# Optimization experiments

Hardware: AMD Instinct MI355X
Metric: run time of the kernel (lower is better)

The kernel has to match this reference:

```python
import jax, jax.numpy as jnp
import numpy as np
import math

D_MODEL = 1024
NUM_HEADS = 16
N_GROUP = 4
HEAD_DIM = D_MODEL // NUM_HEADS  # 64
KV_DIM = N_GROUP * HEAD_DIM      # 256
BS, SEQ = 2, 2048


def setup_inputs() -> dict:
    key = jax.random.key(0)
    ks = jax.random.split(key, 7)
    s = 0.02
    return {
        "h": jax.random.normal(ks[0], (BS, SEQ, D_MODEL), dtype=jnp.float32),
        "wq_w": jax.random.normal(ks[1], (D_MODEL, D_MODEL), dtype=jnp.float32) * s,
        "wq_b": jnp.zeros((D_MODEL,), dtype=jnp.float32),
        "wk_w": jax.random.normal(ks[2], (KV_DIM, D_MODEL), dtype=jnp.float32) * s,
        "wk_b": jnp.zeros((KV_DIM,), dtype=jnp.float32),
        "wv_w": jax.random.normal(ks[3], (KV_DIM, D_MODEL), dtype=jnp.float32) * s,
        "wv_b": jnp.zeros((KV_DIM,), dtype=jnp.float32),
    }


def reference(h, wq_w, wq_b, wk_w, wk_b, wv_w, wv_b):
    bs, seq, _ = h.shape
    rep = NUM_HEADS // N_GROUP  # heads per KV group

    # Linear projections (torch Linear: x @ W.T + b)
    q = h @ wq_w.T + wq_b                     # [bs, seq, d_model]
    k = h @ wk_w.T + wk_b                     # [bs, seq, kv_dim]
    v = h @ wv_w.T + wv_b                     # [bs, seq, kv_dim]

    q = q.reshape(bs, seq, NUM_HEADS, HEAD_DIM).transpose(0, 2, 1, 3)  # [b,H,s,d]
    k = k.reshape(bs, seq, N_GROUP, HEAD_DIM)                          # [b,s,G,d]
    v = v.reshape(bs, seq, N_GROUP, HEAD_DIM)
    # torch .repeat(1,1,1,rep).view(...,num_heads,head_dim) maps head h -> group h//rep,
    # identical to repeating each group `rep` times consecutively along the head axis.
    k = jnp.repeat(k, rep, axis=2).transpose(0, 2, 1, 3)               # [b,H,s,d]
    v = jnp.repeat(v, rep, axis=2).transpose(0, 2, 1, 3)               # [b,H,s,d]

    scores = jnp.einsum("bhqd,bhkd->bhqk", q, k) / math.sqrt(HEAD_DIM)
    attn = jax.nn.softmax(scores, axis=-1)
    out = jnp.einsum("bhqk,bhkd->bhqd", attn, v)                       # [b,H,s,d]
    out = out.transpose(0, 2, 1, 3).reshape(bs, seq, NUM_HEADS * HEAD_DIM)
    return out
```

## Files before the change

### kernel.cpp

```cpp
#include <hip/hip_runtime.h>

typedef _Float16 f16;
typedef _Float16 f16x8 __attribute__((ext_vector_type(8)));
typedef _Float16 f16x4 __attribute__((ext_vector_type(4)));
typedef float f32x4 __attribute__((ext_vector_type(4)));

#define MFMA16(a, b, c) __builtin_amdgcn_mfma_f32_16x16x32_f16((a), (b), (c), 0, 0, 0)
#define GLDS16(g, l)                                                        \
    __builtin_amdgcn_global_load_lds(                                       \
        (const __attribute__((address_space(1))) void*)(g),                 \
        (__attribute__((address_space(3))) void*)(l), 16, 0, 0)

#define SEQ 2048
#define DMODEL 1024
#define NH 16
#define NG 4
#define PAD 76
#define QTP 68

__global__ __launch_bounds__(256) void cvt_all(const float* __restrict__ h,
                                               const float* __restrict__ wq,
                                               const float* __restrict__ wk,
                                               const float* __restrict__ wv,
                                               f16* __restrict__ hb, f16* __restrict__ wqb,
                                               f16* __restrict__ wkb, f16* __restrict__ wvb) {
    const int i = blockIdx.x * 256 + threadIdx.x;
    const float* s; f16* d; int off;
    if (i < 1048576)      { s = h;  d = hb;  off = i; }
    else if (i < 1310720) { s = wq; d = wqb; off = i - 1048576; }
    else if (i < 1376256) { s = wk; d = wkb; off = i - 1310720; }
    else                  { s = wv; d = wvb; off = i - 1376256; }
    const float4 v = ((const float4*)s)[off];
    f16x4 p;
    p[0] = (f16)v.x; p[1] = (f16)v.y; p[2] = (f16)v.z; p[3] = (f16)v.w;
    ((f16x4*)d)[off] = p;
}

__global__ __launch_bounds__(256) void kv_gemm(const f16* __restrict__ hA,
                                               const f16* __restrict__ wk,
                                               const f16* __restrict__ wv,
                                               const float* __restrict__ bk,
                                               const float* __restrict__ bv,
                                               f16* __restrict__ Kb,
                                               f16* __restrict__ Vtb) {
    __shared__ __align__(16) f16 As[64 * 32];
    __shared__ __align__(16) f16 Bs[128 * 32];

    const int tid  = threadIdx.x;
    const int lane = tid & 63;
    const int l15  = lane & 15;
    const int l4   = lane >> 4;
    const int wave = tid >> 6;
    const int wm   = (wave >> 1) * 32;
    const int wn   = (wave & 1) * 64;
    const int bx   = blockIdx.x;
    const int m0   = blockIdx.y * 64;

    const int vmode = (bx >= 2);
    const f16* W = vmode ? wv : wk;
    const float* bias = vmode ? bv : bk;
    const int n0 = (bx & 1) * 128;

    const int rowA = tid >> 2;
    const int colA = (tid & 3) * 8;
    const f16* Ag = hA + (size_t)(m0 + rowA) * DMODEL + colA;
    const f16* Bg = W  + (size_t)(n0 + rowA) * DMODEL + colA;
    const int sOff = wave * 512;

    f32x4 acc[2][4];
#pragma unroll
    for (int i = 0; i < 2; i++)
#pragma unroll
        for (int j = 0; j < 4; j++) acc[i][j] = (f32x4)0.0f;

    for (int k0 = 0; k0 < DMODEL; k0 += 32) {
        GLDS16(Ag + k0,         As + sOff);
        GLDS16(Bg + k0,         Bs + sOff);
        GLDS16(Bg + 65536 + k0, Bs + 2048 + sOff);
        __syncthreads();

        f16x8 af[2], bf[4];
#pragma unroll
        for (int i = 0; i < 2; i++)
            af[i] = *(const f16x8*)&As[(wm + i * 16 + l15) * 32 + l4 * 8];
#pragma unroll
        for (int j = 0; j < 4; j++)
            bf[j] = *(const f16x8*)&Bs[(wn + j * 16 + l15) * 32 + l4 * 8];
#pragma unroll
        for (int i = 0; i < 2; i++)
#pragma unroll
            for (int j = 0; j < 4; j++)
                acc[i][j] = MFMA16(af[i], bf[j], acc[i][j]);
        __syncthreads();
    }

#pragma unroll
    for (int i = 0; i < 2; i++) {
        const int mbase = m0 + wm + i * 16 + l4 * 4;
#pragma unroll
        for (int j = 0; j < 4; j++) {
            const int n  = n0 + wn + j * 16 + l15;
            const float bvv = bias[n];
            if (!vmode) {
#pragma unroll
                for (int r = 0; r < 4; r++)
                    Kb[(size_t)(mbase + r) * 256 + n] = (f16)(acc[i][j][r] + bvv);
            } else {
                f16x4 p;
#pragma unroll
                for (int r = 0; r < 4; r++)
                    p[r] = (f16)(acc[i][j][r] + bvv);
                const int bb = mbase >> 11;
                const int s  = mbase & 2047;
                *(f16x4*)&Vtb[((size_t)(bb * 256 + n)) * SEQ + s] = p;
            }
        }
    }
}

__global__ __launch_bounds__(256, 4) void attn_kernel(const f16* __restrict__ hb,
                                                      const f16* __restrict__ wqb,
                                                      const float* __restrict__ bq,
                                                      const f16* __restrict__ Kt,
                                                      const f16* __restrict__ Vt,
                                                      float* __restrict__ out,
                                                      float qscale) {
    __shared__ __align__(16) f16 Ks[64 * PAD];
    __shared__ __align__(16) f16 Vs[64 * PAD];
    __shared__ __align__(16) f16 Ps[64 * PAD];
    __shared__ __align__(16) f16 Qt[64 * QTP];

    const int tid  = threadIdx.x;
    const int lane = tid & 63;
    const int l15  = lane & 15;
    const int l4   = lane >> 4;
    const int wave = tid >> 6;
    const int b    = blockIdx.z;
    const int hh   = blockIdx.y;
    const int g    = hh >> 2;
    const int q0   = blockIdx.x * 64;
    const int qw   = wave * 16;

    {
        const int rowT = tid >> 2;
        const int colT = (tid & 3) * 16;
        const f16* Hg = hb  + (size_t)(b * SEQ + q0 + rowT) * DMODEL + colT;
        const f16* Wg = wqb + (size_t)(hh * 64 + rowT) * DMODEL + colT;

        f32x4 qacc[4];
#pragma unroll
        for (int j = 0; j < 4; j++) qacc[j] = (f32x4)0.0f;

        for (int k0 = 0; k0 < DMODEL; k0 += 64) {
            __syncthreads();
            *(f16x8*)&Ks[rowT * PAD + colT]     = *(const f16x8*)(Hg + k0);
            *(f16x8*)&Ks[rowT * PAD + colT + 8] = *(const f16x8*)(Hg + k0 + 8);
            *(f16x8*)&Vs[rowT * PAD + colT]     = *(const f16x8*)(Wg + k0);
            *(f16x8*)&Vs[rowT * PAD + colT + 8] = *(const f16x8*)(Wg + k0 + 8);
            __syncthreads();

#pragma unroll
            for (int kc = 0; kc < 2; kc++) {
                const f16x8 af = *(const f16x8*)&Ks[(qw + l15) * PAD + kc * 32 + l4 * 8];
#pragma unroll
                for (int j = 0; j < 4; j++) {
                    const f16x8 bf = *(const f16x8*)&Vs[(j * 16 + l15) * PAD + kc * 32 + l4 * 8];
                    qacc[j] = MFMA16(af, bf, qacc[j]);
                }
            }
        }

#pragma unroll
        for (int j = 0; j < 4; j++) {
            const float bv = bq[hh * 64 + j * 16 + l15];
#pragma unroll
            for (int r = 0; r < 4; r++)
                Qt[(qw + l4 * 4 + r) * QTP + j * 16 + l15] = (f16)((qacc[j][r] + bv) * qscale);
        }
    }

    f16x8 qf[2];
#pragma unroll
    for (int kt = 0; kt < 2; kt++)
        qf[kt] = *(const f16x8*)&Qt[(qw + l15) * QTP + kt * 32 + l4 * 8];

    __syncthreads();

    f32x4 oacc[4];
    float lsum[4];
#pragma unroll
    for (int dt = 0; dt < 4; dt++) oacc[dt] = (f32x4)0.0f;
#pragma unroll
    for (int r = 0; r < 4; r++) lsum[r] = 0.0f;

    const int srow = tid >> 2;
    const int sc8  = (tid & 3) * 8;
    const f16* Kg = Kt + (size_t)(b * SEQ + srow) * 256 + g * 64 + sc8;
    const f16* Vg = Vt + (size_t)(b * 256 + g * 64 + srow) * SEQ + sc8;

    for (int kb = 0; kb < SEQ; kb += 64) {
        *(f16x8*)&Ks[srow * PAD + sc8]      = *(const f16x8*)(Kg + (size_t)kb * 256);
        *(f16x8*)&Ks[srow * PAD + 32 + sc8] = *(const f16x8*)(Kg + (size_t)kb * 256 + 32);
        *(f16x8*)&Vs[srow * PAD + sc8]      = *(const f16x8*)(Vg + kb);
        *(f16x8*)&Vs[srow * PAD + 32 + sc8] = *(const f16x8*)(Vg + kb + 32);
        __syncthreads();

        f32x4 sacc[4];
#pragma unroll
        for (int jt = 0; jt < 4; jt++) sacc[jt] = (f32x4)0.0f;
#pragma unroll
        for (int jt = 0; jt < 4; jt++) {
            const f16x8 kf0 = *(const f16x8*)&Ks[(jt * 16 + l15) * PAD + l4 * 8];
            const f16x8 kf1 = *(const f16x8*)&Ks[(jt * 16 + l15) * PAD + 32 + l4 * 8];
            sacc[jt] = MFMA16(qf[0], kf0, sacc[jt]);
            sacc[jt] = MFMA16(qf[1], kf1, sacc[jt]);
        }

#pragma unroll
        for (int jt = 0; jt < 4; jt++)
#pragma unroll
            for (int r = 0; r < 4; r++) {
                const float p = exp2f(sacc[jt][r]);
                lsum[r] += p;
                Ps[(qw + l4 * 4 + r) * PAD + jt * 16 + l15] = (f16)p;
            }

#pragma unroll
        for (int kt = 0; kt < 2; kt++) {
            const f16x8 pf = *(const f16x8*)&Ps[(qw + l15) * PAD + kt * 32 + l4 * 8];
#pragma unroll
            for (int dt = 0; dt < 4; dt++) {
                const f16x8 vf = *(const f16x8*)&Vs[(dt * 16 + l15) * PAD + kt * 32 + l4 * 8];
                oacc[dt] = MFMA16(pf, vf, oacc[dt]);
            }
        }
        __syncthreads();
    }

#pragma unroll
    for (int r = 0; r < 4; r++) {
        float l = lsum[r];
        l += __shfl_xor(l, 1);
        l += __shfl_xor(l, 2);
        l += __shfl_xor(l, 4);
        l += __shfl_xor(l, 8);
        const float inv = 1.0f / l;
        const int q = q0 + qw + l4 * 4 + r;
        float* op = out + ((size_t)(b * SEQ + q)) * DMODEL + hh * 64;
#pragma unroll
        for (int dt = 0; dt < 4; dt++)
            op[dt * 16 + l15] = oacc[dt][r] * inv;
    }
}

extern "C" void kernel_launch(void* const* d_in, const int* in_sizes, int n_in,
                              void* d_out, int out_size, void* d_ws, size_t ws_size,
                              hipStream_t stream) {
    const float* h    = (const float*)d_in[0];
    const float* wq_w = (const float*)d_in[1];
    const float* wq_b = (const float*)d_in[2];
    const float* wk_w = (const float*)d_in[3];
    const float* wk_b = (const float*)d_in[4];
    const float* wv_w = (const float*)d_in[5];
    const float* wv_b = (const float*)d_in[6];
    float* out = (float*)d_out;

    char* ws = (char*)d_ws;
    f16* hb  = (f16*)(ws + 0);
    f16* wqb = (f16*)(ws + 8388608);
    f16* wkb = (f16*)(ws + 10485760);
    f16* wvb = (f16*)(ws + 11010048);
    f16* Kb  = (f16*)(ws + 11534336);
    f16* Vtb = (f16*)(ws + 13631488);

    cvt_all<<<5632, 256, 0, stream>>>(h, wq_w, wk_w, wv_w, hb, wqb, wkb, wvb);

    kv_gemm<<<dim3(4, 64), 256, 0, stream>>>(hb, wkb, wvb, wk_b, wv_b, Kb, Vtb);

    const float qscale = 0.125f * 1.4426950408889634f;
    attn_kernel<<<dim3(32, 16, 2), 256, 0, stream>>>(hb, wqb, wq_b, Kb, Vtb, out, qscale);
}
```

Before: 194.2 us.

## Fuse fp32→fp16 conversion into KV GEMM and merge prep kernels into one launch

Merges the conversion kernel and the K/V projection GEMM into a single launch. GEMM blocks now read fp32 h and Wk/Wv directly, convert them in registers and store fp16 to LDS. Global loads are register-prefetched one k-step ahead, which replaces the async global-to-LDS loads and removes one barrier per iteration. The remaining blocks convert only h and Wq for the attention kernel. This saves a launch and the fp16 K/V weight round trip, but the GEMM blocks now read fp32 (twice the bytes) and do the conversion work inline, running concurrently with the conversion blocks.

```diff
diff --git a/kernel.cpp b/kernel.cpp
--- a/kernel.cpp
+++ b/kernel.cpp
@@ -6,10 +6,6 @@
 typedef float f32x4 __attribute__((ext_vector_type(4)));
 
 #define MFMA16(a, b, c) __builtin_amdgcn_mfma_f32_16x16x32_f16((a), (b), (c), 0, 0, 0)
-#define GLDS16(g, l)                                                        \
-    __builtin_amdgcn_global_load_lds(                                       \
-        (const __attribute__((address_space(1))) void*)(g),                 \
-        (__attribute__((address_space(3))) void*)(l), 16, 0, 0)
 
 #define SEQ 2048
 #define DMODEL 1024
@@ -18,54 +14,59 @@
 #define PAD 76
 #define QTP 68
 
-__global__ __launch_bounds__(256) void cvt_all(const float* __restrict__ h,
-                                               const float* __restrict__ wq,
-                                               const float* __restrict__ wk,
-                                               const float* __restrict__ wv,
-                                               f16* __restrict__ hb, f16* __restrict__ wqb,
-                                               f16* __restrict__ wkb, f16* __restrict__ wvb) {
-    const int i = blockIdx.x * 256 + threadIdx.x;
-    const float* s; f16* d; int off;
-    if (i < 1048576)      { s = h;  d = hb;  off = i; }
-    else if (i < 1310720) { s = wq; d = wqb; off = i - 1048576; }
-    else if (i < 1376256) { s = wk; d = wkb; off = i - 1310720; }
-    else                  { s = wv; d = wvb; off = i - 1376256; }
-    const float4 v = ((const float4*)s)[off];
-    f16x4 p;
-    p[0] = (f16)v.x; p[1] = (f16)v.y; p[2] = (f16)v.z; p[3] = (f16)v.w;
-    ((f16x4*)d)[off] = p;
-}
-
-__global__ __launch_bounds__(256) void kv_gemm(const f16* __restrict__ hA,
-                                               const f16* __restrict__ wk,
-                                               const f16* __restrict__ wv,
-                                               const float* __restrict__ bk,
-                                               const float* __restrict__ bv,
-                                               f16* __restrict__ Kb,
-                                               f16* __restrict__ Vtb) {
+__device__ __forceinline__ f16x8 cvt8(const float4 a, const float4 b) {
+    f16x8 r;
+    r[0] = (f16)a.x; r[1] = (f16)a.y; r[2] = (f16)a.z; r[3] = (f16)a.w;
+    r[4] = (f16)b.x; r[5] = (f16)b.y; r[6] = (f16)b.z; r[7] = (f16)b.w;
+    return r;
+}
+
+__global__ __launch_bounds__(256) void prep_kernel(const float* __restrict__ h,
+                                                   const float* __restrict__ wq,
+                                                   const float* __restrict__ wk,
+                                                   const float* __restrict__ wv,
+                                                   const float* __restrict__ bk,
+                                                   const float* __restrict__ bv,
+                                                   f16* __restrict__ hb,
+                                                   f16* __restrict__ wqb,
+                                                   f16* __restrict__ Kb,
+                                                   f16* __restrict__ Vtb) {
     __shared__ __align__(16) f16 As[64 * 32];
     __shared__ __align__(16) f16 Bs[128 * 32];
 
-    const int tid  = threadIdx.x;
+    const int bid = blockIdx.x;
+    const int tid = threadIdx.x;
+
+    if (bid >= 256) {
+        const int i = (bid - 256) * 256 + tid;
+        const float* s; f16* d; int off;
+        if (i < 1048576) { s = h;  d = hb;  off = i; }
+        else             { s = wq; d = wqb; off = i - 1048576; }
+        const float4 v = ((const float4*)s)[off];
+        f16x4 p;
+        p[0] = (f16)v.x; p[1] = (f16)v.y; p[2] = (f16)v.z; p[3] = (f16)v.w;
+        ((f16x4*)d)[off] = p;
+        return;
+    }
+
     const int lane = tid & 63;
     const int l15  = lane & 15;
     const int l4   = lane >> 4;
     const int wave = tid >> 6;
     const int wm   = (wave >> 1) * 32;
     const int wn   = (wave & 1) * 64;
-    const int bx   = blockIdx.x;
-    const int m0   = blockIdx.y * 64;
+    const int bx   = bid & 3;
+    const int m0   = (bid >> 2) * 64;
 
     const int vmode = (bx >= 2);
-    const f16* W = vmode ? wv : wk;
+    const float* W = vmode ? wv : wk;
     const float* bias = vmode ? bv : bk;
     const int n0 = (bx & 1) * 128;
 
-    const int rowA = tid >> 2;
-    const int colA = (tid & 3) * 8;
-    const f16* Ag = hA + (size_t)(m0 + rowA) * DMODEL + colA;
-    const f16* Bg = W  + (size_t)(n0 + rowA) * DMODEL + colA;
-    const int sOff = wave * 512;
+    const int rowT = tid >> 2;
+    const int colT = (tid & 3) * 8;
+    const float* Ag = h + (size_t)(m0 + rowT) * DMODEL + colT;
+    const float* Bg = W + (size_t)(n0 + rowT) * DMODEL + colT;
 
     f32x4 acc[2][4];
 #pragma unroll
@@ -73,10 +74,28 @@
 #pragma unroll
         for (int j = 0; j < 4; j++) acc[i][j] = (f32x4)0.0f;
 
+    float4 ra[2], rb0[2], rb1[2];
+    ra[0]  = *(const float4*)(Ag);
+    ra[1]  = *(const float4*)(Ag + 4);
+    rb0[0] = *(const float4*)(Bg);
+    rb0[1] = *(const float4*)(Bg + 4);
+    rb1[0] = *(const float4*)(Bg + (size_t)64 * DMODEL);
+    rb1[1] = *(const float4*)(Bg + (size_t)64 * DMODEL + 4);
+
     for (int k0 = 0; k0 < DMODEL; k0 += 32) {
-        GLDS16(Ag + k0,         As + sOff);
-        GLDS16(Bg + k0,         Bs + sOff);
-        GLDS16(Bg + 65536 + k0, Bs + 2048 + sOff);
+        __syncthreads();
+        *(f16x8*)&As[rowT * 32 + colT]        = cvt8(ra[0], ra[1]);
+        *(f16x8*)&Bs[rowT * 32 + colT]        = cvt8(rb0[0], rb0[1]);
+        *(f16x8*)&Bs[(rowT + 64) * 32 + colT] = cvt8(rb1[0], rb1[1]);
+        if (k0 + 32 < DMODEL) {
+            const int kn = k0 + 32;
+            ra[0]  = *(const float4*)(Ag + kn);
+            ra[1]  = *(const float4*)(Ag + kn + 4);
+            rb0[0] = *(const float4*)(Bg + kn);
+            rb0[1] = *(const float4*)(Bg + kn + 4);
+            rb1[0] = *(const float4*)(Bg + (size_t)64 * DMODEL + kn);
+            rb1[1] = *(const float4*)(Bg + (size_t)64 * DMODEL + kn + 4);
+        }
         __syncthreads();
 
         f16x8 af[2], bf[4];
@@ -91,7 +110,6 @@
 #pragma unroll
             for (int j = 0; j < 4; j++)
                 acc[i][j] = MFMA16(af[i], bf[j], acc[i][j]);
-        __syncthreads();
     }
 
 #pragma unroll
@@ -268,14 +286,11 @@
     char* ws = (char*)d_ws;
     f16* hb  = (f16*)(ws + 0);
     f16* wqb = (f16*)(ws + 8388608);
-    f16* wkb = (f16*)(ws + 10485760);
-    f16* wvb = (f16*)(ws + 11010048);
-    f16* Kb  = (f16*)(ws + 11534336);
-    f16* Vtb = (f16*)(ws + 13631488);
-
-    cvt_all<<<5632, 256, 0, stream>>>(h, wq_w, wk_w, wv_w, hb, wqb, wkb, wvb);
-
-    kv_gemm<<<dim3(4, 64), 256, 0, stream>>>(hb, wkb, wvb, wk_b, wv_b, Kb, Vtb);
+    f16* Kb  = (f16*)(ws + 10485760);
+    f16* Vtb = (f16*)(ws + 12582912);
+
+    prep_kernel<<<dim3(5376), 256, 0, stream>>>(h, wq_w, wk_w, wv_w, wk_b, wv_b,
+                                                hb, wqb, Kb, Vtb);
 
     const float qscale = 0.125f * 1.4426950408889634f;
     attn_kernel<<<dim3(32, 16, 2), 256, 0, stream>>>(hb, wqb, wq_b, Kb, Vtb, out, qscale);
```

Result: no change. 194.6 us (+0.2%).
